# Optimization experiments

Hardware: AMD Instinct MI355X
Metric: run time of the kernel (lower is better)

## Reference

```python
import jax, jax.numpy as jnp
import numpy as np

B, H, W, C = 16, 64, 64, 256
NH = 8
KD = C // NH  # 32
SCALE = KD ** -0.5


def rotate_every_two(x):
    x1 = x[..., ::2]
    x2 = x[..., 1::2]
    return jnp.stack([-x2, x1], axis=-1).reshape(x.shape)


def theta_shift(x, sin, cos):
    return x * cos + rotate_every_two(x) * sin


def dwconv2d(x, w, b):
    # x: (b,h,w,c), w: (5,5,1,c) HWIO depthwise, pad 2
    y = jax.lax.conv_general_dilated(
        x, w, window_strides=(1, 1), padding=((2, 2), (2, 2)),
        dimension_numbers=("NHWC", "HWIO", "NHWC"), feature_group_count=x.shape[-1])
    return y + b


def setup_inputs() -> dict:
    key = jax.random.key(0)
    ks = jax.random.split(key, 12)
    s = 0.02
    return {
        "x": jax.random.normal(ks[0], (B, H, W, C), jnp.float32),
        "sin": jax.random.uniform(ks[1], (H, W, KD), jnp.float32, -1.0, 1.0),
        "cos": jax.random.uniform(ks[2], (H, W, KD), jnp.float32, -1.0, 1.0),
        "mask_h": jax.random.normal(ks[3], (NH, H, H), jnp.float32) * 0.1,
        "mask_w": jax.random.normal(ks[4], (NH, W, W), jnp.float32) * 0.1,
        "Wq": jax.random.normal(ks[5], (C, C), jnp.float32) * s,
        "bq": jnp.zeros((C,), jnp.float32),
        "Wk": jax.random.normal(ks[6], (C, C), jnp.float32) * s,
        "bk": jnp.zeros((C,), jnp.float32),
        "Wv": jax.random.normal(ks[7], (C, C), jnp.float32) * s,
        "bv": jnp.zeros((C,), jnp.float32),
        "conv_w": jax.random.normal(ks[8], (5, 5, 1, C), jnp.float32) * s,
        "conv_b": jnp.zeros((C,), jnp.float32),
        "Wo": jax.random.normal(ks[9], (C, C), jnp.float32) * s,
        "bo": jnp.zeros((C,), jnp.float32),
    }


def reference(x, sin, cos, mask_h, mask_w, Wq, bq, Wk, bk, Wv, bv, conv_w, conv_b, Wo, bo):
    b, h, w, _ = x.shape
    n = mask_w.shape[0]
    kd = sin.shape[-1]

    q = x @ Wq + bq
    k = (x @ Wk + bk) * SCALE
    v = x @ Wv + bv
    lepe = dwconv2d(v, conv_w, conv_b)

    # (b,n,h,w,d)
    q = q.reshape(b, h, w, n, kd).transpose(0, 3, 1, 2, 4)
    k = k.reshape(b, h, w, n, kd).transpose(0, 3, 1, 2, 4)
    qr = theta_shift(q, sin, cos)
    kr = theta_shift(k, sin, cos)

    # width attention: rows independent
    qk_w = jnp.einsum("bhnwd,bhnvd->bhnwv", qr.transpose(0, 2, 1, 3, 4), kr.transpose(0, 2, 1, 3, 4))
    qk_w = jax.nn.softmax(qk_w + mask_w, axis=-1)
    vv = v.reshape(b, h, w, n, -1).transpose(0, 1, 3, 2, 4)  # (b,h,n,w,d2)
    vv = jnp.einsum("bhnwv,bhnvd->bhnwd", qk_w, vv)

    # height attention: columns independent
    qr_h = qr.transpose(0, 3, 1, 2, 4)  # (b,w,n,h,d)
    kr_h = kr.transpose(0, 3, 1, 2, 4)
    vv = vv.transpose(0, 3, 2, 1, 4)  # (b,w,n,h,d2)
    qk_h = jnp.einsum("bwnhd,bwngd->bwnhg", qr_h, kr_h)
    qk_h = jax.nn.softmax(qk_h + mask_h, axis=-1)
    out = jnp.einsum("bwnhg,bwngd->bwnhd", qk_h, vv)

    out = out.transpose(0, 3, 1, 2, 4).reshape(b, h, w, -1)  # (b,h,w,n*d2)
    out = out + lepe
    return out @ Wo + bo
```

## Files before the change

### kernel.cpp

```cpp
#include <hip/hip_runtime.h>

typedef __attribute__((ext_vector_type(8))) short bf16x8;
typedef __attribute__((ext_vector_type(4))) float f32x4;

constexpr int B  = 16;
constexpr int H  = 64;
constexpr int W  = 64;
constexpr int C  = 256;
constexpr int NH = 8;
constexpr int KD = 32;
constexpr float SCALE = 0.17677669529663687f;
constexpr int M_TOT = B * H * W;
constexpr size_t NEL = (size_t)B * H * W * C;

__device__ __forceinline__ unsigned short f2bf(float f) {
    union { float f; unsigned int u; } x; x.f = f;
    unsigned int u = x.u;
    unsigned int r = (u + 0x7fffu + ((u >> 16) & 1u)) >> 16;
    return (unsigned short)r;
}
__device__ __forceinline__ float bf2f(unsigned short s) {
    union { unsigned int u; float f; } x; x.u = ((unsigned int)s) << 16; return x.f;
}
__device__ __forceinline__ float bf_lo(unsigned int u) {
    union { unsigned int u; float f; } x; x.u = u << 16; return x.f;
}
__device__ __forceinline__ float bf_hi(unsigned int u) {
    union { unsigned int u; float f; } x; x.u = u & 0xffff0000u; return x.f;
}
__device__ __forceinline__ unsigned int pack2(float a, float b) {
    return (unsigned int)f2bf(a) | ((unsigned int)f2bf(b) << 16);
}
__device__ __forceinline__ void cvt8(uint4 rv, float* f) {
    f[0] = bf_lo(rv.x); f[1] = bf_hi(rv.x); f[2] = bf_lo(rv.y); f[3] = bf_hi(rv.y);
    f[4] = bf_lo(rv.z); f[5] = bf_hi(rv.z); f[6] = bf_lo(rv.w); f[7] = bf_hi(rv.w);
}
__device__ __forceinline__ int swz(int row, int kp8) {
    return row * 32 + (kp8 ^ (((row >> 2) & 3) << 3));
}

__global__ __launch_bounds__(256) void prep_x16(const float* __restrict__ x,
                                                unsigned short* __restrict__ x16) {
    size_t i8 = ((size_t)blockIdx.x * 256 + threadIdx.x) * 8;
    float4 f0 = *(const float4*)(x + i8);
    float4 f1 = *(const float4*)(x + i8 + 4);
    uint4 o;
    o.x = pack2(f0.x, f0.y); o.y = pack2(f0.z, f0.w);
    o.z = pack2(f1.x, f1.y); o.w = pack2(f1.z, f1.w);
    *(uint4*)(x16 + i8) = o;
}

__global__ __launch_bounds__(256) void trans_all(
    const float* __restrict__ Wq, const float* __restrict__ Wk,
    const float* __restrict__ Wv, const float* __restrict__ Wo,
    unsigned short* __restrict__ dst) {
    int tidg = blockIdx.x * 256 + threadIdx.x;
    int mat = tidg >> 13;
    int lt  = tidg & 8191;
    int n = lt >> 5, k0 = (lt & 31) << 3;
    const float* __restrict__ src = (mat == 0) ? Wq : (mat == 1) ? Wk : (mat == 2) ? Wv : Wo;
    unsigned int p[4];
#pragma unroll
    for (int j = 0; j < 4; ++j) {
        float a  = src[(size_t)(k0 + 2 * j) * 256 + n];
        float b2 = src[(size_t)(k0 + 2 * j + 1) * 256 + n];
        p[j] = pack2(a, b2);
    }
    uint4 o = {p[0], p[1], p[2], p[3]};
    *(uint4*)(dst + ((size_t)mat * 65536) + (size_t)n * 256 + k0) = o;
}

__global__ __launch_bounds__(256) void qkv_mfma(
    const unsigned short* __restrict__ x16, const unsigned short* __restrict__ Wt16,
    const float* __restrict__ bq, const float* __restrict__ bk, const float* __restrict__ bv,
    const float* __restrict__ sin_t, const float* __restrict__ cos_t,
    unsigned short* __restrict__ qr, unsigned short* __restrict__ kr,
    unsigned short* __restrict__ v16)
{
    __shared__ __align__(16) unsigned short As[128 * 32];
    __shared__ __align__(16) unsigned short Bs[128 * 32];

    const int t = threadIdx.x;
    const int lane = t & 63, wid = t >> 6;
    const int wr = wid >> 1, wc = wid & 1;
    const int m0 = blockIdx.x * 128;
    const int n0 = blockIdx.y * 128;
    const int matid = blockIdx.y >> 1;
    const int nb = n0 & 255;

    f32x4 acc[4][4];
#pragma unroll
    for (int i = 0; i < 4; ++i)
#pragma unroll
        for (int j = 0; j < 4; ++j)
#pragma unroll
            for (int q = 0; q < 4; ++q) acc[i][j][q] = 0.f;

    const int row_s = t >> 2;
    const int kp_s  = (t & 3) << 3;

    for (int ks = 0; ks < 8; ++ks) {
        const int k0 = ks * 32;
        const unsigned short* ap = x16 + (size_t)(m0 + row_s) * 256 + k0 + kp_s;
        uint4 a0 = *(const uint4*)ap;
        uint4 a1 = *(const uint4*)(ap + 64 * 256);
        const unsigned short* bp = Wt16 + (size_t)(n0 + row_s) * 256 + k0 + kp_s;
        uint4 b0 = *(const uint4*)bp;
        uint4 b1 = *(const uint4*)(bp + 64 * 256);

        __syncthreads();
        *(uint4*)(&As[swz(row_s,      kp_s)]) = a0;
        *(uint4*)(&As[swz(row_s + 64, kp_s)]) = a1;
        *(uint4*)(&Bs[swz(row_s,      kp_s)]) = b0;
        *(uint4*)(&Bs[swz(row_s + 64, kp_s)]) = b1;
        __syncthreads();

        bf16x8 af[4], bf[4];
        const int rsel = lane & 15, kg8 = (lane >> 4) << 3;
#pragma unroll
        for (int i = 0; i < 4; ++i)
            af[i] = *(const bf16x8*)(&As[swz(wr * 64 + i * 16 + rsel, kg8)]);
#pragma unroll
        for (int j = 0; j < 4; ++j)
            bf[j] = *(const bf16x8*)(&Bs[swz(wc * 64 + j * 16 + rsel, kg8)]);
#pragma unroll
        for (int i = 0; i < 4; ++i)
#pragma unroll
            for (int j = 0; j < 4; ++j)
                acc[i][j] = __builtin_amdgcn_mfma_f32_16x16x32_bf16(bf[j], af[i], acc[i][j], 0, 0, 0);
    }

    const int col_l = lane & 15, rowg = (lane >> 4) << 2;
    if (matid == 2) {
#pragma unroll
        for (int i = 0; i < 4; ++i) {
            const int m = m0 + wr * 64 + i * 16 + col_l;
#pragma unroll
            for (int j = 0; j < 4; ++j) {
                const int nn = nb + wc * 64 + j * 16 + rowg;
                float4 bias4 = *(const float4*)(bv + nn);
                ushort4 o;
                o.x = f2bf(acc[i][j][0] + bias4.x);
                o.y = f2bf(acc[i][j][1] + bias4.y);
                o.z = f2bf(acc[i][j][2] + bias4.z);
                o.w = f2bf(acc[i][j][3] + bias4.w);
                *(ushort4*)(v16 + (size_t)m * 256 + nn) = o;
            }
        }
    } else {
        const float sc = matid ? SCALE : 1.0f;
        const float* __restrict__ bias = matid ? bk : bq;
        unsigned short* __restrict__ dst = matid ? kr : qr;
#pragma unroll
        for (int i = 0; i < 4; ++i) {
            const int m = m0 + wr * 64 + i * 16 + col_l;
            const int bb = m >> 12, hh = (m >> 6) & 63, ww = m & 63;
            const size_t pixbase = ((size_t)hh * 64 + ww) * 32;
#pragma unroll
            for (int j = 0; j < 4; ++j) {
                const int n = nb + wc * 64 + j * 16 + rowg;
                const int nh = n >> 5, db = n & 31;
                float4 bias4 = *(const float4*)(bias + n);
                float4 cs4 = *(const float4*)(cos_t + pixbase + db);
                float4 sn4 = *(const float4*)(sin_t + pixbase + db);
                float v0 = (acc[i][j][0] + bias4.x) * sc;
                float v1 = (acc[i][j][1] + bias4.y) * sc;
                float v2 = (acc[i][j][2] + bias4.z) * sc;
                float v3 = (acc[i][j][3] + bias4.w) * sc;
                ushort4 o;
                o.x = f2bf(v0 * cs4.x - v1 * sn4.x);
                o.y = f2bf(v1 * cs4.y + v0 * sn4.y);
                o.z = f2bf(v2 * cs4.z - v3 * sn4.z);
                o.w = f2bf(v3 * cs4.w + v2 * sn4.w);
                *(ushort4*)(dst + ((((size_t)bb * 8 + nh) * 64 + hh) * 64 + ww) * 32 + db) = o;
            }
        }
    }
}

__global__ __launch_bounds__(256) void conv_kernel(
    const unsigned short* __restrict__ v, const float* __restrict__ cw,
    const float* __restrict__ cb, unsigned short* __restrict__ lepe)
{
    size_t tid = (size_t)blockIdx.x * 256 + threadIdx.x;
    const int c8 = (int)(tid & 31) << 3;
    const int w0 = ((int)(tid >> 5) & 15) << 2;
    const int h  = (int)(tid >> 9) & 63;
    const int b  = (int)(tid >> 15);

    float acc[4][8];
    {
        float4 cb0 = *(const float4*)(cb + c8);
        float4 cb1 = *(const float4*)(cb + c8 + 4);
#pragma unroll
        for (int o = 0; o < 4; ++o) {
            acc[o][0] = cb0.x; acc[o][1] = cb0.y; acc[o][2] = cb0.z; acc[o][3] = cb0.w;
            acc[o][4] = cb1.x; acc[o][5] = cb1.y; acc[o][6] = cb1.z; acc[o][7] = cb1.w;
        }
    }

    const unsigned short* __restrict__ vb = v + (size_t)b * 4096 * 256 + c8;
#pragma unroll
    for (int dy = 0; dy < 5; ++dy) {
        const int yy = h + dy - 2;
        if (yy < 0 || yy >= 64) continue;
        float rowf[8][8];
#pragma unroll
        for (int j = 0; j < 8; ++j) {
            const int xx = w0 + j - 2;
            if (xx < 0 || xx >= 64) {
#pragma unroll
                for (int q = 0; q < 8; ++q) rowf[j][q] = 0.f;
            } else {
                uint4 rv = *(const uint4*)(vb + (size_t)(yy * 64 + xx) * 256);
                cvt8(rv, rowf[j]);
            }
        }
#pragma unroll
        for (int dx = 0; dx < 5; ++dx) {
            const float* wp = cw + (dy * 5 + dx) * 256 + c8;
            float4 wv0 = *(const float4*)wp;
            float4 wv1 = *(const float4*)(wp + 4);
#pragma unroll
            for (int o = 0; o < 4; ++o) {
                const float* rf = rowf[dx + o];
                acc[o][0] += rf[0] * wv0.x; acc[o][1] += rf[1] * wv0.y;
                acc[o][2] += rf[2] * wv0.z; acc[o][3] += rf[3] * wv0.w;
                acc[o][4] += rf[4] * wv1.x; acc[o][5] += rf[5] * wv1.y;
                acc[o][6] += rf[6] * wv1.z; acc[o][7] += rf[7] * wv1.w;
            }
        }
    }

    unsigned short* __restrict__ op = lepe + (((size_t)(b * 64 + h) * 64) + w0) * 256 + c8;
#pragma unroll
    for (int o = 0; o < 4; ++o) {
        uint4 ov;
        ov.x = pack2(acc[o][0], acc[o][1]); ov.y = pack2(acc[o][2], acc[o][3]);
        ov.z = pack2(acc[o][4], acc[o][5]); ov.w = pack2(acc[o][6], acc[o][7]);
        *(uint4*)(op + (size_t)o * 256) = ov;
    }
}

template <int AXIS>
__global__ __launch_bounds__(256) void attn_mfma(
    const unsigned short* __restrict__ qr, const unsigned short* __restrict__ kr,
    const unsigned short* __restrict__ vin, const float* __restrict__ mask,
    const unsigned short* __restrict__ addin, unsigned short* __restrict__ outp)
{
    __shared__ __align__(16) short qs[64 * 40];
    __shared__ __align__(16) short ks[64 * 40];
    __shared__ __align__(16) short vt[32 * 72];
    __shared__ __align__(16) short P [64 * 72];

    const int t    = threadIdx.x;
    const int lane = t & 63, wv = t >> 6;
    const int bid  = blockIdx.x;
    const int nh   = bid & 7;
    const int pos  = (bid >> 3) & 63;
    const int b    = bid >> 9;

    size_t qbase, vbase;
    int qstride, vstride;
    if (AXIS == 0) {
        qbase   = ((size_t)(b * 8 + nh) * 64 + pos) * 2048;
        qstride = 32;
        vbase   = ((size_t)(b * 64 + pos) * 64) * 256 + nh * 32;
        vstride = 256;
    } else {
        qbase   = ((size_t)(b * 8 + nh) * 64) * 2048 + pos * 32;
        qstride = 2048;
        vbase   = ((size_t)b * 64 * 64) * 256 + pos * 256 + nh * 32;
        vstride = 16384;
    }

    {
        int row = t >> 2, c8 = (t & 3) << 3;
        uint4 rq = *(const uint4*)(qr + qbase + (size_t)row * qstride + c8);
        *(uint4*)(&qs[row * 40 + c8]) = rq;
        uint4 rk = *(const uint4*)(kr + qbase + (size_t)row * qstride + c8);
        *(uint4*)(&ks[row * 40 + c8]) = rk;
        uint4 rv = *(const uint4*)(vin + vbase + (size_t)row * vstride + c8);
        const unsigned short* pv = (const unsigned short*)&rv;
#pragma unroll
        for (int j = 0; j < 8; ++j) vt[(c8 + j) * 72 + row] = pv[j];
    }
    __syncthreads();

    const int rsel = lane & 15;
    const int kg   = (lane >> 4) << 3;
    const int rowg = (lane >> 4) << 2;

    bf16x8 aq = *(const bf16x8*)(&qs[(wv * 16 + rsel) * 40 + kg]);
    f32x4 s[4];
#pragma unroll
    for (int j = 0; j < 4; ++j) {
        f32x4 z = {0.f, 0.f, 0.f, 0.f};
        bf16x8 bk8 = *(const bf16x8*)(&ks[(j * 16 + rsel) * 40 + kg]);
        s[j] = __builtin_amdgcn_mfma_f32_16x16x32_bf16(aq, bk8, z, 0, 0, 0);
    }

    const float* __restrict__ mrow = mask + (size_t)nh * 4096;
#pragma unroll
    for (int r = 0; r < 4; ++r) {
        const int grow = wv * 16 + rowg + r;
#pragma unroll
        for (int j = 0; j < 4; ++j)
            s[j][r] += mrow[grow * 64 + j * 16 + rsel];
        float mx = fmaxf(fmaxf(s[0][r], s[1][r]), fmaxf(s[2][r], s[3][r]));
        mx = fmaxf(mx, __shfl_xor(mx, 1));
        mx = fmaxf(mx, __shfl_xor(mx, 2));
        mx = fmaxf(mx, __shfl_xor(mx, 4));
        mx = fmaxf(mx, __shfl_xor(mx, 8));
        float e0 = __expf(s[0][r] - mx), e1 = __expf(s[1][r] - mx);
        float e2 = __expf(s[2][r] - mx), e3 = __expf(s[3][r] - mx);
        float sum = e0 + e1 + e2 + e3;
        sum += __shfl_xor(sum, 1);
        sum += __shfl_xor(sum, 2);
        sum += __shfl_xor(sum, 4);
        sum += __shfl_xor(sum, 8);
        float inv = 1.0f / sum;
        P[grow * 72 +      rsel] = f2bf(e0 * inv);
        P[grow * 72 + 16 + rsel] = f2bf(e1 * inv);
        P[grow * 72 + 32 + rsel] = f2bf(e2 * inv);
        P[grow * 72 + 48 + rsel] = f2bf(e3 * inv);
    }
    __syncthreads();

    f32x4 o[2];
#pragma unroll
    for (int n = 0; n < 2; ++n)
#pragma unroll
        for (int q = 0; q < 4; ++q) o[n][q] = 0.f;
#pragma unroll
    for (int kk = 0; kk < 2; ++kk) {
        bf16x8 ap = *(const bf16x8*)(&P[(wv * 16 + rsel) * 72 + kk * 32 + kg]);
#pragma unroll
        for (int n = 0; n < 2; ++n) {
            bf16x8 bv8 = *(const bf16x8*)(&vt[(n * 16 + rsel) * 72 + kk * 32 + kg]);
            o[n] = __builtin_amdgcn_mfma_f32_16x16x32_bf16(ap, bv8, o[n], 0, 0, 0);
        }
    }

#pragma unroll
    for (int n = 0; n < 2; ++n)
#pragma unroll
        for (int r = 0; r < 4; ++r) {
            const int grow = wv * 16 + rowg + r;
            size_t oidx = vbase + (size_t)grow * vstride + n * 16 + rsel;
            float val = o[n][r];
            if (AXIS == 1) val += bf2f(addin[oidx]);
            outp[oidx] = f2bf(val);
        }
}

__global__ __launch_bounds__(256) void gemm_out_mfma(
    const unsigned short* __restrict__ y16, const unsigned short* __restrict__ Wot16,
    const float* __restrict__ bo, float* __restrict__ out)
{
    __shared__ __align__(16) unsigned short As[128 * 32];
    __shared__ __align__(16) unsigned short Bs[128 * 32];

    const int t = threadIdx.x;
    const int lane = t & 63, wid = t >> 6;
    const int wr = wid >> 1, wc = wid & 1;
    const int m0 = blockIdx.x * 128;
    const int n0 = blockIdx.y * 128;

    f32x4 acc[4][4];
#pragma unroll
    for (int i = 0; i < 4; ++i)
#pragma unroll
        for (int j = 0; j < 4; ++j)
#pragma unroll
            for (int q = 0; q < 4; ++q) acc[i][j][q] = 0.f;

    const int row_s = t >> 2;
    const int kp_s  = (t & 3) << 3;

    for (int ks = 0; ks < 8; ++ks) {
        const int k0 = ks * 32;
        const unsigned short* ap = y16 + (size_t)(m0 + row_s) * 256 + k0 + kp_s;
        uint4 a0 = *(const uint4*)ap;
        uint4 a1 = *(const uint4*)(ap + 64 * 256);
        const unsigned short* bp = Wot16 + (size_t)(n0 + row_s) * 256 + k0 + kp_s;
        uint4 b0 = *(const uint4*)bp;
        uint4 b1 = *(const uint4*)(bp + 64 * 256);

        __syncthreads();
        *(uint4*)(&As[swz(row_s,      kp_s)]) = a0;
        *(uint4*)(&As[swz(row_s + 64, kp_s)]) = a1;
        *(uint4*)(&Bs[swz(row_s,      kp_s)]) = b0;
        *(uint4*)(&Bs[swz(row_s + 64, kp_s)]) = b1;
        __syncthreads();

        bf16x8 af[4], bf[4];
        const int rsel = lane & 15, kg8 = (lane >> 4) << 3;
#pragma unroll
        for (int i = 0; i < 4; ++i)
            af[i] = *(const bf16x8*)(&As[swz(wr * 64 + i * 16 + rsel, kg8)]);
#pragma unroll
        for (int j = 0; j < 4; ++j)
            bf[j] = *(const bf16x8*)(&Bs[swz(wc * 64 + j * 16 + rsel, kg8)]);
#pragma unroll
        for (int i = 0; i < 4; ++i)
#pragma unroll
            for (int j = 0; j < 4; ++j)
                acc[i][j] = __builtin_amdgcn_mfma_f32_16x16x32_bf16(af[i], bf[j], acc[i][j], 0, 0, 0);
    }

    const int col_l = lane & 15, rowg = (lane >> 4) << 2;
#pragma unroll
    for (int i = 0; i < 4; ++i)
#pragma unroll
        for (int j = 0; j < 4; ++j) {
            int nn = n0 + wc * 64 + j * 16 + col_l;
            float bias = bo[nn];
#pragma unroll
            for (int r = 0; r < 4; ++r) {
                int m = m0 + wr * 64 + i * 16 + rowg + r;
                out[(size_t)m * 256 + nn] = acc[i][j][r] + bias;
            }
        }
}

extern "C" void kernel_launch(void* const* d_in, const int* in_sizes, int n_in,
                              void* d_out, int out_size, void* d_ws, size_t ws_size,
                              hipStream_t stream) {
    const float* x      = (const float*)d_in[0];
    const float* sin_t  = (const float*)d_in[1];
    const float* cos_t  = (const float*)d_in[2];
    const float* mask_h = (const float*)d_in[3];
    const float* mask_w = (const float*)d_in[4];
    const float* Wq     = (const float*)d_in[5];
    const float* bq     = (const float*)d_in[6];
    const float* Wk     = (const float*)d_in[7];
    const float* bk     = (const float*)d_in[8];
    const float* Wv     = (const float*)d_in[9];
    const float* bv     = (const float*)d_in[10];
    const float* conv_w = (const float*)d_in[11];
    const float* conv_b = (const float*)d_in[12];
    const float* Wo     = (const float*)d_in[13];
    const float* bo     = (const float*)d_in[14];

    unsigned short* ws    = (unsigned short*)d_ws;
    unsigned short* v16   = ws;
    unsigned short* lepe16= v16 + NEL;
    unsigned short* qr16  = lepe16 + NEL;
    unsigned short* kr16  = qr16 + NEL;
    unsigned short* y16   = kr16 + NEL;
    unsigned short* Wt16  = y16 + NEL;
    unsigned short* Wot16 = Wt16 + 768 * 256;

    unsigned short* vv16 = (unsigned short*)d_out;
    unsigned short* x16  = (unsigned short*)d_out + NEL;

    prep_x16<<<(int)(NEL / 2048), 256, 0, stream>>>(x, x16);
    trans_all<<<128, 256, 0, stream>>>(Wq, Wk, Wv, Wo, Wt16);

    qkv_mfma<<<dim3(M_TOT / 128, 6), 256, 0, stream>>>(
        x16, Wt16, bq, bk, bv, sin_t, cos_t, qr16, kr16, v16);

    conv_kernel<<<(int)(NEL / 32 / 256), 256, 0, stream>>>(v16, conv_w, conv_b, lepe16);

    attn_mfma<0><<<B * H * NH, 256, 0, stream>>>(qr16, kr16, v16, mask_w, nullptr, vv16);

    attn_mfma<1><<<B * W * NH, 256, 0, stream>>>(qr16, kr16, vv16, mask_h, lepe16, y16);

    gemm_out_mfma<<<dim3(M_TOT / 128, 2), 256, 0, stream>>>(y16, Wot16, bo, (float*)d_out);
}
```

Before: 240.3 us.

## Merge prep kernels, stage conv rows in LDS, raise MFMA wave priority

Folds the x-to-bf16 conversion and weight transpose into one launch to save a kernel launch. Rewrites the depthwise conv so each block loads a 5-row, 64-channel slab of v into LDS once and reads neighbours from shared memory, instead of each thread issuing redundant global loads. Each thread now computes 2 outputs instead of 4, so the grid has more blocks. Also wraps the attention MFMA sections in s_setprio to favour waves issuing matrix ops.

```diff
diff --git a/kernel.cpp b/kernel.cpp
--- a/kernel.cpp
+++ b/kernel.cpp
@@ -39,35 +39,37 @@
     return row * 32 + (kp8 ^ (((row >> 2) & 3) << 3));
 }
 
-__global__ __launch_bounds__(256) void prep_x16(const float* __restrict__ x,
-                                                unsigned short* __restrict__ x16) {
-    size_t i8 = ((size_t)blockIdx.x * 256 + threadIdx.x) * 8;
-    float4 f0 = *(const float4*)(x + i8);
-    float4 f1 = *(const float4*)(x + i8 + 4);
-    uint4 o;
-    o.x = pack2(f0.x, f0.y); o.y = pack2(f0.z, f0.w);
-    o.z = pack2(f1.x, f1.y); o.w = pack2(f1.z, f1.w);
-    *(uint4*)(x16 + i8) = o;
-}
-
-__global__ __launch_bounds__(256) void trans_all(
+__global__ __launch_bounds__(256) void prep_all(
+    const float* __restrict__ x, unsigned short* __restrict__ x16,
     const float* __restrict__ Wq, const float* __restrict__ Wk,
     const float* __restrict__ Wv, const float* __restrict__ Wo,
-    unsigned short* __restrict__ dst) {
-    int tidg = blockIdx.x * 256 + threadIdx.x;
-    int mat = tidg >> 13;
-    int lt  = tidg & 8191;
-    int n = lt >> 5, k0 = (lt & 31) << 3;
-    const float* __restrict__ src = (mat == 0) ? Wq : (mat == 1) ? Wk : (mat == 2) ? Wv : Wo;
-    unsigned int p[4];
-#pragma unroll
-    for (int j = 0; j < 4; ++j) {
-        float a  = src[(size_t)(k0 + 2 * j) * 256 + n];
-        float b2 = src[(size_t)(k0 + 2 * j + 1) * 256 + n];
-        p[j] = pack2(a, b2);
-    }
-    uint4 o = {p[0], p[1], p[2], p[3]};
-    *(uint4*)(dst + ((size_t)mat * 65536) + (size_t)n * 256 + k0) = o;
+    unsigned short* __restrict__ wdst)
+{
+    int bid = blockIdx.x;
+    if (bid < 8192) {
+        size_t i8 = ((size_t)bid * 256 + threadIdx.x) * 8;
+        float4 f0 = *(const float4*)(x + i8);
+        float4 f1 = *(const float4*)(x + i8 + 4);
+        uint4 o;
+        o.x = pack2(f0.x, f0.y); o.y = pack2(f0.z, f0.w);
+        o.z = pack2(f1.x, f1.y); o.w = pack2(f1.z, f1.w);
+        *(uint4*)(x16 + i8) = o;
+    } else {
+        int tidg = (bid - 8192) * 256 + threadIdx.x;
+        int mat = tidg >> 13;
+        int lt  = tidg & 8191;
+        int n = lt >> 5, k0 = (lt & 31) << 3;
+        const float* __restrict__ src = (mat == 0) ? Wq : (mat == 1) ? Wk : (mat == 2) ? Wv : Wo;
+        unsigned int p[4];
+#pragma unroll
+        for (int j = 0; j < 4; ++j) {
+            float a  = src[(size_t)(k0 + 2 * j) * 256 + n];
+            float b2 = src[(size_t)(k0 + 2 * j + 1) * 256 + n];
+            p[j] = pack2(a, b2);
+        }
+        uint4 o = {p[0], p[1], p[2], p[3]};
+        *(uint4*)(wdst + ((size_t)mat * 65536) + (size_t)n * 256 + k0) = o;
+    }
 }
 
 __global__ __launch_bounds__(256) void qkv_mfma(
@@ -178,67 +180,80 @@
     }
 }
 
-__global__ __launch_bounds__(256) void conv_kernel(
+__global__ __launch_bounds__(256) void conv_lds(
     const unsigned short* __restrict__ v, const float* __restrict__ cw,
     const float* __restrict__ cb, unsigned short* __restrict__ lepe)
 {
-    size_t tid = (size_t)blockIdx.x * 256 + threadIdx.x;
-    const int c8 = (int)(tid & 31) << 3;
-    const int w0 = ((int)(tid >> 5) & 15) << 2;
-    const int h  = (int)(tid >> 9) & 63;
-    const int b  = (int)(tid >> 15);
-
-    float acc[4][8];
+    __shared__ __align__(16) unsigned short vs[5][64][72];
+
+    const int bid = blockIdx.x;
+    const int cq = bid & 3;
+    const int h  = (bid >> 2) & 63;
+    const int b  = bid >> 8;
+    const int t  = threadIdx.x;
+    const int cg = t & 7;
+    const int c8 = cg << 3;
+    const int cbase = cq * 64 + c8;
+    const int wpair = t >> 3;
+    const int w0 = wpair << 1;
+
+    for (int i = t; i < 2560; i += 256) {
+        const int scg = i & 7, sw = (i >> 3) & 63, sdy = i >> 9;
+        const int yy = h + sdy - 2;
+        uint4 val = {0u, 0u, 0u, 0u};
+        if (yy >= 0 && yy < 64)
+            val = *(const uint4*)(v + ((size_t)(b * 64 + yy) * 64 + sw) * 256 + cq * 64 + scg * 8);
+        *(uint4*)(&vs[sdy][sw][scg * 8]) = val;
+    }
+    __syncthreads();
+
+    float acc[2][8];
     {
-        float4 cb0 = *(const float4*)(cb + c8);
-        float4 cb1 = *(const float4*)(cb + c8 + 4);
-#pragma unroll
-        for (int o = 0; o < 4; ++o) {
-            acc[o][0] = cb0.x; acc[o][1] = cb0.y; acc[o][2] = cb0.z; acc[o][3] = cb0.w;
-            acc[o][4] = cb1.x; acc[o][5] = cb1.y; acc[o][6] = cb1.z; acc[o][7] = cb1.w;
-        }
-    }
-
-    const unsigned short* __restrict__ vb = v + (size_t)b * 4096 * 256 + c8;
+        float4 cb0 = *(const float4*)(cb + cbase);
+        float4 cb1 = *(const float4*)(cb + cbase + 4);
+#pragma unroll
+        for (int wi = 0; wi < 2; ++wi) {
+            acc[wi][0] = cb0.x; acc[wi][1] = cb0.y; acc[wi][2] = cb0.z; acc[wi][3] = cb0.w;
+            acc[wi][4] = cb1.x; acc[wi][5] = cb1.y; acc[wi][6] = cb1.z; acc[wi][7] = cb1.w;
+        }
+    }
+
 #pragma unroll
     for (int dy = 0; dy < 5; ++dy) {
-        const int yy = h + dy - 2;
-        if (yy < 0 || yy >= 64) continue;
-        float rowf[8][8];
-#pragma unroll
-        for (int j = 0; j < 8; ++j) {
-            const int xx = w0 + j - 2;
+        float rowf[6][8];
+#pragma unroll
+        for (int e = 0; e < 6; ++e) {
+            const int xx = w0 + e - 2;
             if (xx < 0 || xx >= 64) {
 #pragma unroll
-                for (int q = 0; q < 8; ++q) rowf[j][q] = 0.f;
+                for (int q = 0; q < 8; ++q) rowf[e][q] = 0.f;
             } else {
-                uint4 rv = *(const uint4*)(vb + (size_t)(yy * 64 + xx) * 256);
-                cvt8(rv, rowf[j]);
+                uint4 rv = *(const uint4*)(&vs[dy][xx][c8]);
+                cvt8(rv, rowf[e]);
             }
         }
 #pragma unroll
         for (int dx = 0; dx < 5; ++dx) {
-            const float* wp = cw + (dy * 5 + dx) * 256 + c8;
+            const float* wp = cw + (dy * 5 + dx) * 256 + cbase;
             float4 wv0 = *(const float4*)wp;
             float4 wv1 = *(const float4*)(wp + 4);
 #pragma unroll
-            for (int o = 0; o < 4; ++o) {
-                const float* rf = rowf[dx + o];
-                acc[o][0] += rf[0] * wv0.x; acc[o][1] += rf[1] * wv0.y;
-                acc[o][2] += rf[2] * wv0.z; acc[o][3] += rf[3] * wv0.w;
-                acc[o][4] += rf[4] * wv1.x; acc[o][5] += rf[5] * wv1.y;
-                acc[o][6] += rf[6] * wv1.z; acc[o][7] += rf[7] * wv1.w;
+            for (int wi = 0; wi < 2; ++wi) {
+                const float* rf = rowf[dx + wi];
+                acc[wi][0] += rf[0] * wv0.x; acc[wi][1] += rf[1] * wv0.y;
+                acc[wi][2] += rf[2] * wv0.z; acc[wi][3] += rf[3] * wv0.w;
+                acc[wi][4] += rf[4] * wv1.x; acc[wi][5] += rf[5] * wv1.y;
+                acc[wi][6] += rf[6] * wv1.z; acc[wi][7] += rf[7] * wv1.w;
             }
         }
     }
 
-    unsigned short* __restrict__ op = lepe + (((size_t)(b * 64 + h) * 64) + w0) * 256 + c8;
-#pragma unroll
-    for (int o = 0; o < 4; ++o) {
+#pragma unroll
+    for (int wi = 0; wi < 2; ++wi) {
         uint4 ov;
-        ov.x = pack2(acc[o][0], acc[o][1]); ov.y = pack2(acc[o][2], acc[o][3]);
-        ov.z = pack2(acc[o][4], acc[o][5]); ov.w = pack2(acc[o][6], acc[o][7]);
-        *(uint4*)(op + (size_t)o * 256) = ov;
+        ov.x = pack2(acc[wi][0], acc[wi][1]); ov.y = pack2(acc[wi][2], acc[wi][3]);
+        ov.z = pack2(acc[wi][4], acc[wi][5]); ov.w = pack2(acc[wi][6], acc[wi][7]);
+        *(uint4*)(lepe + ((size_t)(b * 64 + h) * 64 + w0 + wi) * 256 + cbase) = ov;
     }
 }
 
@@ -293,12 +308,14 @@
 
     bf16x8 aq = *(const bf16x8*)(&qs[(wv * 16 + rsel) * 40 + kg]);
     f32x4 s[4];
+    __builtin_amdgcn_s_setprio(1);
 #pragma unroll
     for (int j = 0; j < 4; ++j) {
         f32x4 z = {0.f, 0.f, 0.f, 0.f};
         bf16x8 bk8 = *(const bf16x8*)(&ks[(j * 16 + rsel) * 40 + kg]);
         s[j] = __builtin_amdgcn_mfma_f32_16x16x32_bf16(aq, bk8, z, 0, 0, 0);
     }
+    __builtin_amdgcn_s_setprio(0);
 
     const float* __restrict__ mrow = mask + (size_t)nh * 4096;
 #pragma unroll
@@ -332,6 +349,7 @@
     for (int n = 0; n < 2; ++n)
 #pragma unroll
         for (int q = 0; q < 4; ++q) o[n][q] = 0.f;
+    __builtin_amdgcn_s_setprio(1);
 #pragma unroll
     for (int kk = 0; kk < 2; ++kk) {
         bf16x8 ap = *(const bf16x8*)(&P[(wv * 16 + rsel) * 72 + kk * 32 + kg]);
@@ -341,6 +359,7 @@
             o[n] = __builtin_amdgcn_mfma_f32_16x16x32_bf16(ap, bv8, o[n], 0, 0, 0);
         }
     }
+    __builtin_amdgcn_s_setprio(0);
 
 #pragma unroll
     for (int n = 0; n < 2; ++n)
@@ -455,13 +474,12 @@
     unsigned short* vv16 = (unsigned short*)d_out;
     unsigned short* x16  = (unsigned short*)d_out + NEL;
 
-    prep_x16<<<(int)(NEL / 2048), 256, 0, stream>>>(x, x16);
-    trans_all<<<128, 256, 0, stream>>>(Wq, Wk, Wv, Wo, Wt16);
+    prep_all<<<8192 + 128, 256, 0, stream>>>(x, x16, Wq, Wk, Wv, Wo, Wt16);
 
     qkv_mfma<<<dim3(M_TOT / 128, 6), 256, 0, stream>>>(
         x16, Wt16, bq, bk, bv, sin_t, cos_t, qr16, kr16, v16);
 
-    conv_kernel<<<(int)(NEL / 32 / 256), 256, 0, stream>>>(v16, conv_w, conv_b, lepe16);
+    conv_lds<<<B * H * 4, 256, 0, stream>>>(v16, conv_w, conv_b, lepe16);
 
     attn_mfma<0><<<B * H * NH, 256, 0, stream>>>(qr16, kr16, v16, mask_w, nullptr, vv16);
 
```

After: 316.1 us. 31.6% more time.
